# Kernel tuning notes

Measured on AMD Instinct MI355X. Metric: run time of the kernel, lower is better.

The kernel has to match this reference:

```python
import jax, jax.numpy as jnp
import numpy as np

N, E, B = 100000, 1600000, 512
NE, EE, H = 32, 32, 64
SCALE = float(2**48 - 1)


def _mlp2(x, W1, b1, W2, b2):
    # Linear -> ReLU -> Linear
    return jax.nn.relu(x @ W1 + b1) @ W2 + b2


def _gine(x, src, dst, e, W1, b1, W2, b2, n):
    # GINEConv (eps=0): nn(x + sum_j relu(x_j + e_ij))
    m = jax.nn.relu(x[src] + e)                      # [E, d] gather + edge add
    agg = jax.ops.segment_sum(m, dst, num_segments=n)  # scatter-add to targets
    return _mlp2(x + agg, W1, b1, W2, b2)


def _encode(names, edge_index, edge_attr, batch,
            idW1, idb1, idW2, idb2, edW1, edb1, edW2, edb2,
            c1W1, c1b1, c1W2, c1b2, c2W1, c2b1, c2W2, c2b2, linW, linb):
    norm = jnp.clip((names.astype(jnp.float32) + 2.0) / SCALE, 0.0, 1.0)[:, None]
    x = _mlp2(norm, idW1, idb1, idW2, idb2)          # [N, NE]
    e = _mlp2(edge_attr, edW1, edb1, edW2, edb2)     # [E, EE]
    src, dst = edge_index[0], edge_index[1]
    x = jax.nn.relu(_gine(x, src, dst, e, c1W1, c1b1, c1W2, c1b2, N))
    e2 = e @ linW + linb                             # edge lin for conv2 (EE->H)
    x = jax.nn.relu(_gine(x, src, dst, e2, c2W1, c2b1, c2W2, c2b2, N))
    sums = jax.ops.segment_sum(x, batch, num_segments=B)
    cnt = jax.ops.segment_sum(jnp.ones((x.shape[0],), x.dtype), batch, num_segments=B)
    return sums / jnp.maximum(cnt, 1.0)[:, None]     # global_mean_pool


def setup_inputs() -> dict:
    key = jax.random.key(0)
    ks = iter(jax.random.split(key, 64))
    def w(shape):
        return jax.random.normal(next(ks), shape, dtype=jnp.float32) * 0.05
    d = {}
    d['node_names_s'] = jax.random.randint(next(ks), (N,), 0, 1000000)
    d['edge_index_s'] = jax.random.randint(next(ks), (2, E), 0, N)
    d['edge_attr_s'] = jax.random.uniform(next(ks), (E, 1), dtype=jnp.float32)
    d['batch_s'] = jnp.sort(jax.random.randint(next(ks), (N,), 0, B))
    d['node_names_g'] = jax.random.randint(next(ks), (N,), 0, 1000000)
    d['edge_index_g'] = jax.random.randint(next(ks), (2, E), 0, N)
    d['edge_attr_g'] = jax.random.uniform(next(ks), (E, 1), dtype=jnp.float32)
    d['batch_g'] = jnp.sort(jax.random.randint(next(ks), (N,), 0, B))
    d['depth'] = jax.random.uniform(next(ks), (B,), dtype=jnp.float32)
    # shared encoders
    d['idW1'], d['idb1'], d['idW2'], d['idb2'] = w((1, NE)), w((NE,)), w((NE, NE)), w((NE,))
    d['edW1'], d['edb1'], d['edW2'], d['edb2'] = w((1, EE)), w((EE,)), w((EE, EE)), w((EE,))
    # state convs
    d['s1W1'], d['s1b1'], d['s1W2'], d['s1b2'] = w((NE, H)), w((H,)), w((H, H)), w((H,))
    d['s2W1'], d['s2b1'], d['s2W2'], d['s2b2'] = w((H, H)), w((H,)), w((H, H)), w((H,))
    d['s2linW'], d['s2linb'] = w((EE, H)), w((H,))
    # goal convs
    d['g1W1'], d['g1b1'], d['g1W2'], d['g1b2'] = w((NE, H)), w((H,)), w((H, H)), w((H,))
    d['g2W1'], d['g2b1'], d['g2W2'], d['g2b2'] = w((H, H)), w((H,)), w((H, H)), w((H,))
    d['g2linW'], d['g2linb'] = w((EE, H)), w((H,))
    d['rW1'], d['rb1'], d['rW2'], d['rb2'] = w((2 * H + 1, H)), w((H,)), w((H, 1)), w((1,))
    return d


def reference(node_names_s, edge_index_s, edge_attr_s, batch_s,
              node_names_g, edge_index_g, edge_attr_g, batch_g, depth,
              idW1, idb1, idW2, idb2, edW1, edb1, edW2, edb2,
              s1W1, s1b1, s1W2, s1b2, s2W1, s2b1, s2W2, s2b2, s2linW, s2linb,
              g1W1, g1b1, g1W2, g1b2, g2W1, g2b1, g2W2, g2b2, g2linW, g2linb,
              rW1, rb1, rW2, rb2):
    s = _encode(node_names_s, edge_index_s, edge_attr_s, batch_s,
                idW1, idb1, idW2, idb2, edW1, edb1, edW2, edb2,
                s1W1, s1b1, s1W2, s1b2, s2W1, s2b1, s2W2, s2b2, s2linW, s2linb)
    g = _encode(node_names_g, edge_index_g, edge_attr_g, batch_g,
                idW1, idb1, idW2, idb2, edW1, edb1, edW2, edb2,
                g1W1, g1b1, g1W2, g1b2, g2W1, g2b1, g2W2, g2b2, g2linW, g2linb)
    z = jnp.concatenate([s, g, depth[:, None]], axis=1)  # [B, 2H+1]
    return _mlp2(z, rW1, rb1, rW2, rb2)[:, 0]            # [B]
```

## Files before the change

### kernel.cpp

```cpp
#include <hip/hip_runtime.h>
#include <hip/hip_fp16.h>
#include <stdint.h>

namespace {

constexpr int NN   = 100000;
constexpr int TN   = 2 * NN;
constexpr int NEDG = 1600000;
constexpr int TE   = 2 * NEDG;
constexpr int NBAT = 512;
constexpr int NSEG = 33;

constexpr int NC     = 782;
constexpr int TILE   = 4096;
constexpr int ABLK   = (TE + TILE - 1) / TILE;
constexpr int ENTCAP = 5120;

constexpr int S1H = 20;
constexpr int S2H = 36;

constexpr int TAB_BP = 0;
constexpr int TAB_D1 = 32;
constexpr int TAB_C1 = TAB_D1 + NSEG * 32;
constexpr int TAB_E2 = TAB_C1 + NSEG * 32;
constexpr int TAB_TOTAL = TAB_E2 + 4 * NSEG * 64;

__device__ __forceinline__ float relu_(float x) { return fmaxf(x, 0.0f); }

__device__ __forceinline__ float4 shfl_xor4(float4 v, int m) {
  return make_float4(__shfl_xor(v.x, m), __shfl_xor(v.y, m),
                     __shfl_xor(v.z, m), __shfl_xor(v.w, m));
}

__device__ __forceinline__ __half2 bch(int u) {
  return *reinterpret_cast<__half2*>(&u);
}
__device__ __forceinline__ int f2h2(float a, float b) {
  __half2 h = __floats2half2_rn(a, b);
  return *reinterpret_cast<int*>(&h);
}

__global__ void build_tables(const float* __restrict__ eW1, const float* __restrict__ eb1,
                             const float* __restrict__ eW2, const float* __restrict__ eb2,
                             const float* __restrict__ sLW, const float* __restrict__ sLb,
                             const float* __restrict__ gLW, const float* __restrict__ gLb,
                             float* __restrict__ tabs) {
  __shared__ float traw[32];
  __shared__ float ts[32];
  __shared__ float dt[NSEG * 32];
  __shared__ float ct[NSEG * 32];
  int tid = threadIdx.x;
  if (tid < 32) {
    float w = eW1[tid], b = eb1[tid];
    traw[tid] = (w != 0.0f) ? (-b / w) : 3.0e38f;
  }
  __syncthreads();
  if (tid < 32) {
    float v = traw[tid];
    int r = 0;
    for (int j = 0; j < 32; ++j) {
      float u = traw[j];
      r += (u < v) || (u == v && j < tid);
    }
    ts[r] = v;
  }
  __syncthreads();
  if (tid < 32) tabs[TAB_BP + tid] = ts[tid];
  for (int idx = tid; idx < NSEG * 32; idx += blockDim.x) {
    int s = idx >> 5, j = idx & 31;
    float a;
    if (s == 0)            a = ts[0] - 1.0f;
    else if (s == NSEG - 1) a = ts[31] + 1.0f;
    else                   a = 0.5f * ts[s - 1] + 0.5f * ts[s];
    float d = 0.0f, c = 0.0f;
    for (int i = 0; i < 32; ++i) {
      float w = eW1[i], b = eb1[i];
      if (fmaf(a, w, b) > 0.0f) {
        float w2 = eW2[i * 32 + j];
        d = fmaf(w, w2, d);
        c = fmaf(b, w2, c);
      }
    }
    c += eb2[j];
    dt[idx] = d; ct[idx] = c;
    tabs[TAB_D1 + idx] = d;
    tabs[TAB_C1 + idx] = c;
  }
  __syncthreads();
  for (int idx = tid; idx < NSEG * 64; idx += blockDim.x) {
    int s = idx >> 6, k = idx & 63;
    float ds = 0.f, cs = 0.f, dg = 0.f, cg = 0.f;
    for (int j = 0; j < 32; ++j) {
      float dv = dt[s * 32 + j], cv = ct[s * 32 + j];
      float ws = sLW[j * 64 + k], wg = gLW[j * 64 + k];
      ds = fmaf(dv, ws, ds); cs = fmaf(cv, ws, cs);
      dg = fmaf(dv, wg, dg); cg = fmaf(cv, wg, cg);
    }
    cs += sLb[k]; cg += gLb[k];
    tabs[TAB_E2 + idx]                 = ds;
    tabs[TAB_E2 + NSEG * 64 + idx]     = cs;
    tabs[TAB_E2 + 2 * NSEG * 64 + idx] = dg;
    tabs[TAB_E2 + 3 * NSEG * 64 + idx] = cg;
  }
}

__global__ __launch_bounds__(256) void fused_front(
    const int* __restrict__ names_s, const int* __restrict__ names_g,
    const float* __restrict__ idW1, const float* __restrict__ idb1,
    const float* __restrict__ idW2, const float* __restrict__ idb2,
    const int* __restrict__ src_s, const int* __restrict__ dst_s, const float* __restrict__ attr_s,
    const int* __restrict__ src_g, const int* __restrict__ dst_g, const float* __restrict__ attr_g,
    const int* __restrict__ bat_s, const int* __restrict__ bat_g,
    const float* __restrict__ tabs,
    float* __restrict__ x0, __half* __restrict__ x0h,
    int* __restrict__ gcur, int2* __restrict__ part,
    int* __restrict__ start_s, int* __restrict__ start_g) {
  __shared__ int hist[NC];
  __shared__ int lofs[NC];
  __shared__ int lcur[NC];
  __shared__ int2 sorted[TILE];
  __shared__ int addr[TILE];
  __shared__ int scanbuf[256];
  __shared__ float bp[32];
  int t = threadIdx.x;
  if (blockIdx.x < ABLK) {
    if (t < 32) bp[t] = tabs[TAB_BP + t];
    for (int i = t; i < NC; i += 256) hist[i] = 0;
    __syncthreads();
    int base = blockIdx.x * TILE;
#pragma unroll
    for (int j = 0; j < 16; ++j) {
      int i = base + j * 256 + t;
      if (i < TE) {
        int d = (i < NEDG) ? dst_s[i] : (dst_g[i - NEDG] + NN);
        atomicAdd(&hist[d >> 8], 1);
      }
    }
    __syncthreads();
    int loc[4];
    int sum = 0;
#pragma unroll
    for (int j = 0; j < 4; ++j) {
      int b = t * 4 + j;
      int v = (b < NC) ? hist[b] : 0;
      loc[j] = sum; sum += v;
    }
    scanbuf[t] = sum;
    __syncthreads();
    for (int st = 1; st < 256; st <<= 1) {
      int u = (t >= st) ? scanbuf[t - st] : 0;
      __syncthreads();
      scanbuf[t] += u;
      __syncthreads();
    }
    int texcl = scanbuf[t] - sum;
#pragma unroll
    for (int j = 0; j < 4; ++j) {
      int b = t * 4 + j;
      if (b < NC) { lofs[b] = texcl + loc[j]; lcur[b] = 0; }
    }
    __syncthreads();
    for (int b = t; b < NC; b += 256) {
      int c = hist[b];
      hist[b] = c ? atomicAdd(&gcur[b], c) : 0;
    }
    __syncthreads();
#pragma unroll
    for (int j = 0; j < 16; ++j) {
      int i = base + j * 256 + t;
      if (i < TE) {
        int sl, d; float a;
        if (i < NEDG) { sl = src_s[i]; d = dst_s[i]; a = attr_s[i]; }
        else { int k = i - NEDG; sl = src_g[k]; d = dst_g[k] + NN; a = attr_g[k]; }
        int seg = 0;
#pragma unroll
        for (int q = 0; q < 32; ++q) seg += (bp[q] < a);
        int c = d >> 8;
        int r = atomicAdd(&lcur[c], 1);
        int s = lofs[c] + r;
        sorted[s] = make_int2(sl | ((d & 255) << 17) | (seg << 25), __float_as_int(a));
        addr[s] = c * ENTCAP + hist[c] + r;
      }
    }
    __syncthreads();
    int tot = (base + TILE <= TE) ? TILE : (TE - base);
    for (int s = t; s < tot; s += 256) part[addr[s]] = sorted[s];
  } else if (blockIdx.x < ABLK + 782) {
    int n = (blockIdx.x - ABLK) * 256 + t;
    if (n >= TN) return;
    int name = (n < NN) ? names_s[n] : names_g[n - NN];
    float norm = ((float)name + 2.0f) / 281474976710655.0f;
    norm = fminf(fmaxf(norm, 0.0f), 1.0f);
    float h[32];
#pragma unroll
    for (int i = 0; i < 32; ++i) h[i] = relu_(fmaf(norm, idW1[i], idb1[i]));
    float4* out = (float4*)(x0 + (size_t)n * 32);
    int2* outh = (int2*)(x0h + (size_t)n * 32);
    for (int j0 = 0; j0 < 32; j0 += 4) {
      float a0 = idb2[j0], a1 = idb2[j0 + 1], a2 = idb2[j0 + 2], a3 = idb2[j0 + 3];
#pragma unroll
      for (int i = 0; i < 32; ++i) {
        float hv = h[i];
        a0 = fmaf(hv, idW2[i * 32 + j0],     a0);
        a1 = fmaf(hv, idW2[i * 32 + j0 + 1], a1);
        a2 = fmaf(hv, idW2[i * 32 + j0 + 2], a2);
        a3 = fmaf(hv, idW2[i * 32 + j0 + 3], a3);
      }
      out[j0 >> 2] = make_float4(a0, a1, a2, a3);
      outh[j0 >> 2] = make_int2(f2h2(a0, a1), f2h2(a2, a3));
    }
  } else {
    int blk = blockIdx.x - ABLK - 782;
    int half = blk >= 391;
    const int* bat = half ? bat_g : bat_s;
    int* start = half ? start_g : start_s;
    int i = (blk - half * 391) * 256 + t;
    if (i >= NN) return;
    int cur = bat[i];
    int prev = (i == 0) ? -1 : bat[i - 1];
    for (int b = prev + 1; b <= cur; ++b) start[b] = i;
    if (i == NN - 1) {
      for (int b = cur + 1; b <= NBAT; ++b) start[b] = NN;
    }
  }
}

__global__ __launch_bounds__(1024) void coarse_scan(
    const int* __restrict__ gcur, int* __restrict__ cbase, int* __restrict__ rowptr) {
  __shared__ int s[1024];
  int t = threadIdx.x;
  int v = (t < NC) ? min(gcur[t], ENTCAP) : 0;
  s[t] = v;
  __syncthreads();
  for (int st = 1; st < 1024; st <<= 1) {
    int u = (t >= st) ? s[t - st] : 0;
    __syncthreads();
    s[t] += u;
    __syncthreads();
  }
  if (t < NC) cbase[t] = s[t] - v;
  if (t == 0) rowptr[TN] = TE;
}

__global__ __launch_bounds__(256) void partition_to_csr(
    const int* __restrict__ gcur, const int* __restrict__ cbase,
    const int2* __restrict__ part,
    int* __restrict__ rowptr, int2* __restrict__ colattr) {
  __shared__ int2 outE[ENTCAP];
  __shared__ int hist[256];
  __shared__ int cur[256];
  __shared__ int sc[256];
  int t = threadIdx.x, b = blockIdx.x;
  hist[t] = 0;
  __syncthreads();
  int cnt = min(gcur[b], ENTCAP);
  int ibase = b * ENTCAP;
  int obase = cbase[b];
  for (int i = t; i < cnt; i += 256)
    atomicAdd(&hist[(part[ibase + i].x >> 17) & 255], 1);
  __syncthreads();
  int v = hist[t];
  sc[t] = v;
  __syncthreads();
  for (int st = 1; st < 256; st <<= 1) {
    int u = (t >= st) ? sc[t - st] : 0;
    __syncthreads();
    sc[t] += u;
    __syncthreads();
  }
  int excl = sc[t] - v;
  int gnode = b * 256 + t;
  if (gnode < TN) rowptr[gnode] = obase + excl;
  cur[t] = excl;
  __syncthreads();
  for (int i = t; i < cnt; i += 256) {
    int2 e = part[ibase + i];
    int dl = (e.x >> 17) & 255;
    int srcn = e.x & 0x1FFFF;
    int seg = (e.x >> 25) & 63;
    int pos = atomicAdd(&cur[dl], 1);
    outE[pos] = make_int2(srcn | (seg << 20), e.y);
  }
  __syncthreads();
  for (int i = t; i < cnt; i += 256) colattr[obase + i] = outE[i];
}

__global__ __launch_bounds__(256) void conv1_dual(
    const float* __restrict__ x0, const __half* __restrict__ x0h,
    const int* __restrict__ rowptr, const int2* __restrict__ colattr,
    const float* __restrict__ tabs, float* __restrict__ hb) {
  __shared__ __half2 dt2[NSEG * S1H];
  __shared__ __half2 ct2[NSEG * S1H];
  for (int i = threadIdx.x; i < NSEG * 16; i += 256) {
    int s = i >> 4, j = i & 15;
    dt2[s * S1H + j] = __floats2half2_rn(tabs[TAB_D1 + s * 32 + 2 * j],
                                         tabs[TAB_D1 + s * 32 + 2 * j + 1]);
    ct2[s * S1H + j] = __floats2half2_rn(tabs[TAB_C1 + s * 32 + 2 * j],
                                         tabs[TAB_C1 + s * 32 + 2 * j + 1]);
  }
  __syncthreads();
  int n = blockIdx.x * 4 + (threadIdx.x >> 6);
  const __half* xb = x0h + (n >= NN ? (size_t)NN * 32 : 0);
  int lane = threadIdx.x & 63;
  int sub = lane & 7;
  int f0  = (lane >> 3) * 4;
  int h0  = (lane >> 3) * 2;
  int beg = rowptr[n], end = rowptr[n + 1];
  float4 acc = make_float4(0.f, 0.f, 0.f, 0.f);
  for (int k = beg + sub; k < end; k += 16) {
    int2 ca0 = colattr[k];
    int kb = k + 8;
    bool has1 = kb < end;
    int2 ca1 = has1 ? colattr[kb] : ca0;
    unsigned p0 = (unsigned)ca0.x, p1 = (unsigned)ca1.x;
    int s0 = (int)(p0 & 0xFFFFFu), g0 = (int)(p0 >> 20);
    int s1 = (int)(p1 & 0xFFFFFu), g1 = (int)(p1 >> 20);
    float a0 = __int_as_float(ca0.y), a1 = __int_as_float(ca1.y);
    __half2 az0 = __floats2half2_rn(a0, a0);
    __half2 az1 = __floats2half2_rn(a1, a1);
    int2 xv0 = *(const int2*)(xb + (size_t)s0 * 32 + f0);
    int2 xv1 = *(const int2*)(xb + (size_t)s1 * 32 + f0);
    int2 dv0 = *(const int2*)&dt2[g0 * S1H + h0];
    int2 cv0 = *(const int2*)&ct2[g0 * S1H + h0];
    __half2 v;
    float2 f;
    v = __hadd2(bch(xv0.x), __hfma2(az0, bch(dv0.x), bch(cv0.x)));
    f = __half22float2(v); acc.x += relu_(f.x); acc.y += relu_(f.y);
    v = __hadd2(bch(xv0.y), __hfma2(az0, bch(dv0.y), bch(cv0.y)));
    f = __half22float2(v); acc.z += relu_(f.x); acc.w += relu_(f.y);
    if (has1) {
      int2 dv1 = *(const int2*)&dt2[g1 * S1H + h0];
      int2 cv1 = *(const int2*)&ct2[g1 * S1H + h0];
      v = __hadd2(bch(xv1.x), __hfma2(az1, bch(dv1.x), bch(cv1.x)));
      f = __half22float2(v); acc.x += relu_(f.x); acc.y += relu_(f.y);
      v = __hadd2(bch(xv1.y), __hfma2(az1, bch(dv1.y), bch(cv1.y)));
      f = __half22float2(v); acc.z += relu_(f.x); acc.w += relu_(f.y);
    }
  }
#pragma unroll
  for (int m = 1; m < 8; m <<= 1) {
    float4 o = shfl_xor4(acc, m);
    acc.x += o.x; acc.y += o.y; acc.z += o.z; acc.w += o.w;
  }
  if (sub == 0) {
    const float4 self = *(const float4*)(x0 + (size_t)n * 32 + f0);
    *(float4*)(hb + (size_t)n * 32 + f0) =
        make_float4(self.x + acc.x, self.y + acc.y, self.z + acc.z, self.w + acc.w);
  }
}

__global__ __launch_bounds__(256) void conv2_dual(
    const float* __restrict__ x1, const __half* __restrict__ x1h,
    const int* __restrict__ rowptr, const int2* __restrict__ colattr,
    const float* __restrict__ tabs, float* __restrict__ hb) {
  __shared__ __half2 dt2[NSEG * S2H];
  __shared__ __half2 ct2[NSEG * S2H];
  int half = blockIdx.x >= (NN / 4);
  const float* d2 = tabs + TAB_E2 + (size_t)half * 2 * NSEG * 64;
  for (int i = threadIdx.x; i < NSEG * 32; i += 256) {
    int s = i >> 5, j = i & 31;
    dt2[s * S2H + j] = __floats2half2_rn(d2[s * 64 + 2 * j], d2[s * 64 + 2 * j + 1]);
    ct2[s * S2H + j] = __floats2half2_rn(d2[NSEG * 64 + s * 64 + 2 * j],
                                         d2[NSEG * 64 + s * 64 + 2 * j + 1]);
  }
  __syncthreads();
  int n = blockIdx.x * 4 + (threadIdx.x >> 6);
  const __half* xb = x1h + (size_t)half * NN * 64;
  int lane = threadIdx.x & 63;
  int sub = lane & 7;
  int f0  = (lane >> 3) * 8;
  int h0  = (lane >> 3) * 4;
  int beg = rowptr[n], end = rowptr[n + 1];
  float4 accA = make_float4(0.f, 0.f, 0.f, 0.f);
  float4 accB = make_float4(0.f, 0.f, 0.f, 0.f);
  for (int k = beg + sub; k < end; k += 16) {
    int2 ca0 = colattr[k];
    int kb = k + 8;
    bool has1 = kb < end;
    int2 ca1 = has1 ? colattr[kb] : ca0;
    unsigned p0 = (unsigned)ca0.x, p1 = (unsigned)ca1.x;
    int s0 = (int)(p0 & 0xFFFFFu), g0 = (int)(p0 >> 20);
    int s1 = (int)(p1 & 0xFFFFFu), g1 = (int)(p1 >> 20);
    float a0 = __int_as_float(ca0.y), a1 = __int_as_float(ca1.y);
    __half2 az0 = __floats2half2_rn(a0, a0);
    __half2 az1 = __floats2half2_rn(a1, a1);
    int4 xv0 = *(const int4*)(xb + (size_t)s0 * 64 + f0);
    int4 xv1 = *(const int4*)(xb + (size_t)s1 * 64 + f0);
    int4 dv0 = *(const int4*)&dt2[g0 * S2H + h0];
    int4 cv0 = *(const int4*)&ct2[g0 * S2H + h0];
    __half2 v;
    float2 f;
    v = __hadd2(bch(xv0.x), __hfma2(az0, bch(dv0.x), bch(cv0.x)));
    f = __half22float2(v); accA.x += relu_(f.x); accA.y += relu_(f.y);
    v = __hadd2(bch(xv0.y), __hfma2(az0, bch(dv0.y), bch(cv0.y)));
    f = __half22float2(v); accA.z += relu_(f.x); accA.w += relu_(f.y);
    v = __hadd2(bch(xv0.z), __hfma2(az0, bch(dv0.z), bch(cv0.z)));
    f = __half22float2(v); accB.x += relu_(f.x); accB.y += relu_(f.y);
    v = __hadd2(bch(xv0.w), __hfma2(az0, bch(dv0.w), bch(cv0.w)));
    f = __half22float2(v); accB.z += relu_(f.x); accB.w += relu_(f.y);
    if (has1) {
      int4 dv1 = *(const int4*)&dt2[g1 * S2H + h0];
      int4 cv1 = *(const int4*)&ct2[g1 * S2H + h0];
      v = __hadd2(bch(xv1.x), __hfma2(az1, bch(dv1.x), bch(cv1.x)));
      f = __half22float2(v); accA.x += relu_(f.x); accA.y += relu_(f.y);
      v = __hadd2(bch(xv1.y), __hfma2(az1, bch(dv1.y), bch(cv1.y)));
      f = __half22float2(v); accA.z += relu_(f.x); accA.w += relu_(f.y);
      v = __hadd2(bch(xv1.z), __hfma2(az1, bch(dv1.z), bch(cv1.z)));
      f = __half22float2(v); accB.x += relu_(f.x); accB.y += relu_(f.y);
      v = __hadd2(bch(xv1.w), __hfma2(az1, bch(dv1.w), bch(cv1.w)));
      f = __half22float2(v); accB.z += relu_(f.x); accB.w += relu_(f.y);
    }
  }
#pragma unroll
  for (int m = 1; m < 8; m <<= 1) {
    float4 oA = shfl_xor4(accA, m);
    float4 oB = shfl_xor4(accB, m);
    accA.x += oA.x; accA.y += oA.y; accA.z += oA.z; accA.w += oA.w;
    accB.x += oB.x; accB.y += oB.y; accB.z += oB.z; accB.w += oB.w;
  }
  if (sub == 0) {
    const float* sp = x1 + (size_t)n * 64 + f0;
    const float4 sA = *(const float4*)sp;
    const float4 sB = *(const float4*)(sp + 4);
    float* op = hb + (size_t)n * 64 + f0;
    *(float4*)op       = make_float4(sA.x + accA.x, sA.y + accA.y, sA.z + accA.z, sA.w + accA.w);
    *(float4*)(op + 4) = make_float4(sB.x + accB.x, sB.y + accB.y, sB.z + accB.z, sB.w + accB.w);
  }
}

__global__ __launch_bounds__(256) void mlp1_dual(
    const float* __restrict__ hin,
    const float* __restrict__ sW1, const float* __restrict__ sb1,
    const float* __restrict__ sW2, const float* __restrict__ sb2,
    const float* __restrict__ gW1, const float* __restrict__ gb1,
    const float* __restrict__ gW2, const float* __restrict__ gb2,
    float* __restrict__ xout, __half* __restrict__ hout) {
  constexpr int IN = 32;
  __shared__ float hsT[IN][65];
  __shared__ float ysT[64][65];
  int base = blockIdx.x * 64;
  for (int idx = threadIdx.x; idx < 64 * IN; idx += 256) {
    int node = idx / IN, k = idx - node * IN;
    hsT[k][node] = hin[(size_t)(base + node) * IN + k];
  }
  __syncthreads();
  int nt = threadIdx.x >> 4, jx = threadIdx.x & 15;
  int n0 = nt * 4, f0 = jx * 4;
  bool isg = (base + n0) >= NN;
  const float* W1 = isg ? gW1 : sW1;
  const float* b1 = isg ? gb1 : sb1;
  const float* W2 = isg ? gW2 : sW2;
  const float* b2 = isg ? gb2 : sb2;
  float4 acc0, acc1, acc2, acc3;
  {
    const float4 b = *(const float4*)(b1 + f0);
    acc0 = b; acc1 = b; acc2 = b; acc3 = b;
  }
  for (int k = 0; k < IN; ++k) {
    const float4 h = *(const float4*)&hsT[k][n0];
    const float4 w = *(const float4*)(W1 + k * 64 + f0);
    acc0.x = fmaf(h.x, w.x, acc0.x); acc0.y = fmaf(h.x, w.y, acc0.y);
    acc0.z = fmaf(h.x, w.z, acc0.z); acc0.w = fmaf(h.x, w.w, acc0.w);
    acc1.x = fmaf(h.y, w.x, acc1.x); acc1.y = fmaf(h.y, w.y, acc1.y);
    acc1.z = fmaf(h.y, w.z, acc1.z); acc1.w = fmaf(h.y, w.w, acc1.w);
    acc2.x = fmaf(h.z, w.x, acc2.x); acc2.y = fmaf(h.z, w.y, acc2.y);
    acc2.z = fmaf(h.z, w.z, acc2.z); acc2.w = fmaf(h.z, w.w, acc2.w);
    acc3.x = fmaf(h.w, w.x, acc3.x); acc3.y = fmaf(h.w, w.y, acc3.y);
    acc3.z = fmaf(h.w, w.z, acc3.z); acc3.w = fmaf(h.w, w.w, acc3.w);
  }
  ysT[f0 + 0][n0 + 0] = relu_(acc0.x); ysT[f0 + 1][n0 + 0] = relu_(acc0.y);
  ysT[f0 + 2][n0 + 0] = relu_(acc0.z); ysT[f0 + 3][n0 + 0] = relu_(acc0.w);
  ysT[f0 + 0][n0 + 1] = relu_(acc1.x); ysT[f0 + 1][n0 + 1] = relu_(acc1.y);
  ysT[f0 + 2][n0 + 1] = relu_(acc1.z); ysT[f0 + 3][n0 + 1] = relu_(acc1.w);
  ysT[f0 + 0][n0 + 2] = relu_(acc2.x); ysT[f0 + 1][n0 + 2] = relu_(acc2.y);
  ysT[f0 + 2][n0 + 2] = relu_(acc2.z); ysT[f0 + 3][n0 + 2] = relu_(acc2.w);
  ysT[f0 + 0][n0 + 3] = relu_(acc3.x); ysT[f0 + 1][n0 + 3] = relu_(acc3.y);
  ysT[f0 + 2][n0 + 3] = relu_(acc3.z); ysT[f0 + 3][n0 + 3] = relu_(acc3.w);
  __syncthreads();
  {
    const float4 b = *(const float4*)(b2 + f0);
    acc0 = b; acc1 = b; acc2 = b; acc3 = b;
  }
  for (int k = 0; k < 64; ++k) {
    const float4 h = *(const float4*)&ysT[k][n0];
    const float4 w = *(const float4*)(W2 + k * 64 + f0);
    acc0.x = fmaf(h.x, w.x, acc0.x); acc0.y = fmaf(h.x, w.y, acc0.y);
    acc0.z = fmaf(h.x, w.z, acc0.z); acc0.w = fmaf(h.x, w.w, acc0.w);
    acc1.x = fmaf(h.y, w.x, acc1.x); acc1.y = fmaf(h.y, w.y, acc1.y);
    acc1.z = fmaf(h.y, w.z, acc1.z); acc1.w = fmaf(h.y, w.w, acc1.w);
    acc2.x = fmaf(h.z, w.x, acc2.x); acc2.y = fmaf(h.z, w.y, acc2.y);
    acc2.z = fmaf(h.z, w.z, acc2.z); acc2.w = fmaf(h.z, w.w, acc2.w);
    acc3.x = fmaf(h.w, w.x, acc3.x); acc3.y = fmaf(h.w, w.y, acc3.y);
    acc3.z = fmaf(h.w, w.z, acc3.z); acc3.w = fmaf(h.w, w.w, acc3.w);
  }
  float4 o;
  o = make_float4(relu_(acc0.x), relu_(acc0.y), relu_(acc0.z), relu_(acc0.w));
  *(float4*)(xout + (size_t)(base + n0 + 0) * 64 + f0) = o;
  *(int2*)(hout + (size_t)(base + n0 + 0) * 64 + f0) = make_int2(f2h2(o.x, o.y), f2h2(o.z, o.w));
  o = make_float4(relu_(acc1.x), relu_(acc1.y), relu_(acc1.z), relu_(acc1.w));
  *(float4*)(xout + (size_t)(base + n0 + 1) * 64 + f0) = o;
  *(int2*)(hout + (size_t)(base + n0 + 1) * 64 + f0) = make_int2(f2h2(o.x, o.y), f2h2(o.z, o.w));
  o = make_float4(relu_(acc2.x), relu_(acc2.y), relu_(acc2.z), relu_(acc2.w));
  *(float4*)(xout + (size_t)(base + n0 + 2) * 64 + f0) = o;
  *(int2*)(hout + (size_t)(base + n0 + 2) * 64 + f0) = make_int2(f2h2(o.x, o.y), f2h2(o.z, o.w));
  o = make_float4(relu_(acc3.x), relu_(acc3.y), relu_(acc3.z), relu_(acc3.w));
  *(float4*)(xout + (size_t)(base + n0 + 3) * 64 + f0) = o;
  *(int2*)(hout + (size_t)(base + n0 + 3) * 64 + f0) = make_int2(f2h2(o.x, o.y), f2h2(o.z, o.w));
}

__global__ __launch_bounds__(256) void mlp2_pool_dual(
    const float* __restrict__ hin,
    const float* __restrict__ sW1, const float* __restrict__ sb1,
    const float* __restrict__ sW2, const float* __restrict__ sb2,
    const float* __restrict__ gW1, const float* __restrict__ gb1,
    const float* __restrict__ gW2, const float* __restrict__ gb2,
    const int* __restrict__ bat_s, const int* __restrict__ bat_g,
    float* __restrict__ psum) {
  constexpr int IN = 64;
  __shared__ float hsT[IN][65];
  __shared__ float ysT[64][65];
  __shared__ int pid[64];
  int base = blockIdx.x * 64;
  for (int idx = threadIdx.x; idx < 64 * IN; idx += 256) {
    int node = idx / IN, k = idx - node * IN;
    hsT[k][node] = hin[(size_t)(base + node) * IN + k];
  }
  if (threadIdx.x < 64) {
    int gb = base + threadIdx.x;
    pid[threadIdx.x] = (gb < NN) ? bat_s[gb] : (NBAT + bat_g[gb - NN]);
  }
  __syncthreads();
  int nt = threadIdx.x >> 4, jx = threadIdx.x & 15;
  int n0 = nt * 4, f0 = jx * 4;
  bool isg = (base + n0) >= NN;
  const float* W1 = isg ? gW1 : sW1;
  const float* b1 = isg ? gb1 : sb1;
  const float* W2 = isg ? gW2 : sW2;
  const float* b2 = isg ? gb2 : sb2;
  float4 acc0, acc1, acc2, acc3;
  {
    const float4 b = *(const float4*)(b1 + f0);
    acc0 = b; acc1 = b; acc2 = b; acc3 = b;
  }
  for (int k = 0; k < IN; ++k) {
    const float4 h = *(const float4*)&hsT[k][n0];
    const float4 w = *(const float4*)(W1 + k * 64 + f0);
    acc0.x = fmaf(h.x, w.x, acc0.x); acc0.y = fmaf(h.x, w.y, acc0.y);
    acc0.z = fmaf(h.x, w.z, acc0.z); acc0.w = fmaf(h.x, w.w, acc0.w);
    acc1.x = fmaf(h.y, w.x, acc1.x); acc1.y = fmaf(h.y, w.y, acc1.y);
    acc1.z = fmaf(h.y, w.z, acc1.z); acc1.w = fmaf(h.y, w.w, acc1.w);
    acc2.x = fmaf(h.z, w.x, acc2.x); acc2.y = fmaf(h.z, w.y, acc2.y);
    acc2.z = fmaf(h.z, w.z, acc2.z); acc2.w = fmaf(h.z, w.w, acc2.w);
    acc3.x = fmaf(h.w, w.x, acc3.x); acc3.y = fmaf(h.w, w.y, acc3.y);
    acc3.z = fmaf(h.w, w.z, acc3.z); acc3.w = fmaf(h.w, w.w, acc3.w);
  }
  ysT[f0 + 0][n0 + 0] = relu_(acc0.x); ysT[f0 + 1][n0 + 0] = relu_(acc0.y);
  ysT[f0 + 2][n0 + 0] = relu_(acc0.z); ysT[f0 + 3][n0 + 0] = relu_(acc0.w);
  ysT[f0 + 0][n0 + 1] = relu_(acc1.x); ysT[f0 + 1][n0 + 1] = relu_(acc1.y);
  ysT[f0 + 2][n0 + 1] = relu_(acc1.z); ysT[f0 + 3][n0 + 1] = relu_(acc1.w);
  ysT[f0 + 0][n0 + 2] = relu_(acc2.x); ysT[f0 + 1][n0 + 2] = relu_(acc2.y);
  ysT[f0 + 2][n0 + 2] = relu_(acc2.z); ysT[f0 + 3][n0 + 2] = relu_(acc2.w);
  ysT[f0 + 0][n0 + 3] = relu_(acc3.x); ysT[f0 + 1][n0 + 3] = relu_(acc3.y);
  ysT[f0 + 2][n0 + 3] = relu_(acc3.z); ysT[f0 + 3][n0 + 3] = relu_(acc3.w);
  __syncthreads();
  {
    const float4 b = *(const float4*)(b2 + f0);
    acc0 = b; acc1 = b; acc2 = b; acc3 = b;
  }
  for (int k = 0; k < 64; ++k) {
    const float4 h = *(const float4*)&ysT[k][n0];
    const float4 w = *(const float4*)(W2 + k * 64 + f0);
    acc0.x = fmaf(h.x, w.x, acc0.x); acc0.y = fmaf(h.x, w.y, acc0.y);
    acc0.z = fmaf(h.x, w.z, acc0.z); acc0.w = fmaf(h.x, w.w, acc0.w);
    acc1.x = fmaf(h.y, w.x, acc1.x); acc1.y = fmaf(h.y, w.y, acc1.y);
    acc1.z = fmaf(h.y, w.z, acc1.z); acc1.w = fmaf(h.y, w.w, acc1.w);
    acc2.x = fmaf(h.z, w.x, acc2.x); acc2.y = fmaf(h.z, w.y, acc2.y);
    acc2.z = fmaf(h.z, w.z, acc2.z); acc2.w = fmaf(h.z, w.w, acc2.w);
    acc3.x = fmaf(h.w, w.x, acc3.x); acc3.y = fmaf(h.w, w.y, acc3.y);
    acc3.z = fmaf(h.w, w.z, acc3.z); acc3.w = fmaf(h.w, w.w, acc3.w);
  }
  __syncthreads();
  ysT[f0 + 0][n0 + 0] = relu_(acc0.x); ysT[f0 + 1][n0 + 0] = relu_(acc0.y);
  ysT[f0 + 2][n0 + 0] = relu_(acc0.z); ysT[f0 + 3][n0 + 0] = relu_(acc0.w);
  ysT[f0 + 0][n0 + 1] = relu_(acc1.x); ysT[f0 + 1][n0 + 1] = relu_(acc1.y);
  ysT[f0 + 2][n0 + 1] = relu_(acc1.z); ysT[f0 + 3][n0 + 1] = relu_(acc1.w);
  ysT[f0 + 0][n0 + 2] = relu_(acc2.x); ysT[f0 + 1][n0 + 2] = relu_(acc2.y);
  ysT[f0 + 2][n0 + 2] = relu_(acc2.z); ysT[f0 + 3][n0 + 2] = relu_(acc2.w);
  ysT[f0 + 0][n0 + 3] = relu_(acc3.x); ysT[f0 + 1][n0 + 3] = relu_(acc3.y);
  ysT[f0 + 2][n0 + 3] = relu_(acc3.z); ysT[f0 + 3][n0 + 3] = relu_(acc3.w);
  __syncthreads();
  int c = threadIdx.x >> 6, f = threadIdx.x & 63;
  int cur = pid[c * 16];
  float run = 0.0f;
  for (int i = 0; i < 16; ++i) {
    int nx = c * 16 + i;
    int p = pid[nx];
    if (p != cur) { atomicAdd(&psum[(size_t)cur * 64 + f], run); run = 0.0f; cur = p; }
    run += ysT[f][nx];
  }
  atomicAdd(&psum[(size_t)cur * 64 + f], run);
}

__global__ __launch_bounds__(256) void regressor16(
    const float* __restrict__ psum,
    const int* __restrict__ start_s, const int* __restrict__ start_g,
    const float* __restrict__ depth,
    const float* __restrict__ W1, const float* __restrict__ b1,
    const float* __restrict__ W2, const float* __restrict__ b2,
    float* __restrict__ out) {
  __shared__ float zs[16][132];
  __shared__ float ys[64][17];
  __shared__ float inv_s[16], inv_g[16];
  int base = blockIdx.x * 16;
  if (threadIdx.x < 16) {
    int b = base + threadIdx.x;
    inv_s[threadIdx.x] = 1.0f / fmaxf((float)(start_s[b + 1] - start_s[b]), 1.0f);
    inv_g[threadIdx.x] = 1.0f / fmaxf((float)(start_g[b + 1] - start_g[b]), 1.0f);
  }
  __syncthreads();
  for (int i = threadIdx.x; i < 16 * 64; i += 256) {
    int ln = i >> 6, k = i & 63;
    zs[ln][k]      = psum[(size_t)(base + ln) * 64 + k] * inv_s[ln];
    zs[ln][64 + k] = psum[(size_t)(NBAT + base + ln) * 64 + k] * inv_g[ln];
  }
  if (threadIdx.x < 16) zs[threadIdx.x][128] = depth[base + threadIdx.x];
  __syncthreads();
  int g = threadIdx.x >> 4;
  int j = threadIdx.x & 15;
  int f0 = j * 4;
  float a0, a1, a2, a3;
  {
    const float4 b = *(const float4*)(b1 + f0);
    a0 = b.x; a1 = b.y; a2 = b.z; a3 = b.w;
  }
  for (int k = 0; k < 129; ++k) {
    float zv = zs[g][k];
    const float4 w = *(const float4*)(W1 + k * 64 + f0);
    a0 = fmaf(zv, w.x, a0); a1 = fmaf(zv, w.y, a1);
    a2 = fmaf(zv, w.z, a2); a3 = fmaf(zv, w.w, a3);
  }
  ys[f0 + 0][g] = relu_(a0);
  ys[f0 + 1][g] = relu_(a1);
  ys[f0 + 2][g] = relu_(a2);
  ys[f0 + 3][g] = relu_(a3);
  __syncthreads();
  float s = ys[f0 + 0][g] * W2[f0 + 0] + ys[f0 + 1][g] * W2[f0 + 1] +
            ys[f0 + 2][g] * W2[f0 + 2] + ys[f0 + 3][g] * W2[f0 + 3];
#pragma unroll
  for (int m = 1; m < 16; m <<= 1) s += __shfl_xor(s, m);
  if (j == 0) out[base + g] = s + b2[0];
}

}

extern "C" void kernel_launch(void* const* d_in, const int* in_sizes, int n_in,
                              void* d_out, int out_size, void* d_ws, size_t ws_size,
                              hipStream_t stream) {
  const int*   names_s = (const int*)d_in[0];
  const int*   ei_s    = (const int*)d_in[1];
  const float* ea_s    = (const float*)d_in[2];
  const int*   bat_s   = (const int*)d_in[3];
  const int*   names_g = (const int*)d_in[4];
  const int*   ei_g    = (const int*)d_in[5];
  const float* ea_g    = (const float*)d_in[6];
  const int*   bat_g   = (const int*)d_in[7];
  const float* depth   = (const float*)d_in[8];
  const float* idW1 = (const float*)d_in[9],  *idb1 = (const float*)d_in[10];
  const float* idW2 = (const float*)d_in[11], *idb2 = (const float*)d_in[12];
  const float* edW1 = (const float*)d_in[13], *edb1 = (const float*)d_in[14];
  const float* edW2 = (const float*)d_in[15], *edb2 = (const float*)d_in[16];
  const float* s1W1 = (const float*)d_in[17], *s1b1 = (const float*)d_in[18];
  const float* s1W2 = (const float*)d_in[19], *s1b2 = (const float*)d_in[20];
  const float* s2W1 = (const float*)d_in[21], *s2b1 = (const float*)d_in[22];
  const float* s2W2 = (const float*)d_in[23], *s2b2 = (const float*)d_in[24];
  const float* s2LW = (const float*)d_in[25], *s2Lb = (const float*)d_in[26];
  const float* g1W1 = (const float*)d_in[27], *g1b1 = (const float*)d_in[28];
  const float* g1W2 = (const float*)d_in[29], *g1b2 = (const float*)d_in[30];
  const float* g2W1 = (const float*)d_in[31], *g2b1 = (const float*)d_in[32];
  const float* g2W2 = (const float*)d_in[33], *g2b2 = (const float*)d_in[34];
  const float* g2LW = (const float*)d_in[35], *g2Lb = (const float*)d_in[36];
  const float* rW1  = (const float*)d_in[37], *rb1  = (const float*)d_in[38];
  const float* rW2  = (const float*)d_in[39], *rb2  = (const float*)d_in[40];
  (void)in_sizes; (void)n_in; (void)out_size; (void)ws_size;

  char* ws = (char*)d_ws;
  size_t off = 0;
  auto alloc = [&](size_t bytes) -> char* {
    char* p = ws + off;
    off += (bytes + 255) & ~(size_t)255;
    return p;
  };
  float* tabs    = (float*)alloc((size_t)TAB_TOTAL * 4);
  char*  act   = alloc((size_t)TN * 64 * 4 * 2);
  float* x0buf = (float*)act;
  float* h1buf = (float*)(act + (size_t)TN * 32 * 4);
  float* x1buf = (float*)(act + (size_t)TN * 64 * 4);
  int2*  part  = (int2*)x1buf;
  float* h2buf = (float*)act;
  __half* x0h  = (__half*)alloc((size_t)TN * 32 * 2);
  __half* x1h  = (__half*)alloc((size_t)TN * 64 * 2);
  int2*  colattr = (int2*) alloc((size_t)TE * 8);
  int*   gcur    = (int*)  alloc((size_t)NC * 4);
  int*   cbase   = (int*)  alloc((size_t)NC * 4);
  int*   rowptr  = (int*)  alloc((size_t)(TN + 1) * 4);
  int*   start_s = (int*)  alloc((size_t)(NBAT + 1) * 4);
  int*   start_g = (int*)  alloc((size_t)(NBAT + 1) * 4);
  float* psum    = (float*)alloc((size_t)2 * NBAT * 64 * 4);

  build_tables<<<1, 256, 0, stream>>>(edW1, edb1, edW2, edb2, s2LW, s2Lb, g2LW, g2Lb, tabs);
  hipMemsetAsync(gcur, 0, (size_t)NC * 4, stream);
  hipMemsetAsync(psum, 0, (size_t)2 * NBAT * 64 * 4, stream);

  fused_front<<<ABLK + 782 + 782, 256, 0, stream>>>(
      names_s, names_g, idW1, idb1, idW2, idb2,
      ei_s, ei_s + NEDG, ea_s, ei_g, ei_g + NEDG, ea_g,
      bat_s, bat_g, tabs, x0buf, x0h, gcur, part, start_s, start_g);
  coarse_scan<<<1, 1024, 0, stream>>>(gcur, cbase, rowptr);
  partition_to_csr<<<NC, 256, 0, stream>>>(gcur, cbase, part, rowptr, colattr);

  conv1_dual<<<TN / 4, 256, 0, stream>>>(x0buf, x0h, rowptr, colattr, tabs, h1buf);
  mlp1_dual<<<TN / 64, 256, 0, stream>>>(h1buf,
                                         s1W1, s1b1, s1W2, s1b2,
                                         g1W1, g1b1, g1W2, g1b2, x1buf, x1h);
  conv2_dual<<<TN / 4, 256, 0, stream>>>(x1buf, x1h, rowptr, colattr, tabs, h2buf);
  mlp2_pool_dual<<<TN / 64, 256, 0, stream>>>(h2buf,
                                              s2W1, s2b1, s2W2, s2b2,
                                              g2W1, g2b1, g2W2, g2b2,
                                              bat_s, bat_g, psum);
  regressor16<<<32, 256, 0, stream>>>(psum, start_s, start_g, depth,
                                      rW1, rb1, rW2, rb2, (float*)d_out);
}
```

Baseline: 678.1 us.

## Drop fp32 activation copies and widen per-lane gathers in conv kernels

Removes the fp32 copies of x0 and x1; the self term in each conv is now read from the existing fp16 buffers, which cuts global writes and reads. The conv kernels regroup lanes into 16 edge slots times 4 feature groups, so each lane gathers 16 or 32 contiguous bytes per edge instead of 8 or 16. A wave-level __any check skips the second edge slot when no lane has one, and a 0/1 multiplier masks the lanes that do not. The self term is now rounded to fp16, which slightly reduces accuracy, and the wider per-lane accumulators raise register pressure.

```diff
diff --git a/kernel.cpp b/kernel.cpp
--- a/kernel.cpp
+++ b/kernel.cpp
@@ -112,7 +112,7 @@
     const int* __restrict__ src_g, const int* __restrict__ dst_g, const float* __restrict__ attr_g,
     const int* __restrict__ bat_s, const int* __restrict__ bat_g,
     const float* __restrict__ tabs,
-    float* __restrict__ x0, __half* __restrict__ x0h,
+    __half* __restrict__ x0h,
     int* __restrict__ gcur, int2* __restrict__ part,
     int* __restrict__ start_s, int* __restrict__ start_g) {
   __shared__ int hist[NC];
@@ -194,7 +194,6 @@
     float h[32];
 #pragma unroll
     for (int i = 0; i < 32; ++i) h[i] = relu_(fmaf(norm, idW1[i], idb1[i]));
-    float4* out = (float4*)(x0 + (size_t)n * 32);
     int2* outh = (int2*)(x0h + (size_t)n * 32);
     for (int j0 = 0; j0 < 32; j0 += 4) {
       float a0 = idb2[j0], a1 = idb2[j0 + 1], a2 = idb2[j0 + 2], a3 = idb2[j0 + 3];
@@ -206,7 +205,6 @@
         a2 = fmaf(hv, idW2[i * 32 + j0 + 2], a2);
         a3 = fmaf(hv, idW2[i * 32 + j0 + 3], a3);
       }
-      out[j0 >> 2] = make_float4(a0, a1, a2, a3);
       outh[j0 >> 2] = make_int2(f2h2(a0, a1), f2h2(a2, a3));
     }
   } else {
@@ -285,8 +283,24 @@
   for (int i = t; i < cnt; i += 256) colattr[obase + i] = outE[i];
 }
 
+__device__ __forceinline__ void edge_math1(int4 xv, const __half2* dt2, const __half2* ct2,
+                                           int g, int h0, __half2 az, float m,
+                                           float4& A, float4& B) {
+  int4 dv = *(const int4*)&dt2[g * S1H + h0];
+  int4 cv = *(const int4*)&ct2[g * S1H + h0];
+  __half2 v; float2 f;
+  v = __hadd2(bch(xv.x), __hfma2(az, bch(dv.x), bch(cv.x)));
+  f = __half22float2(v); A.x = fmaf(m, relu_(f.x), A.x); A.y = fmaf(m, relu_(f.y), A.y);
+  v = __hadd2(bch(xv.y), __hfma2(az, bch(dv.y), bch(cv.y)));
+  f = __half22float2(v); A.z = fmaf(m, relu_(f.x), A.z); A.w = fmaf(m, relu_(f.y), A.w);
+  v = __hadd2(bch(xv.z), __hfma2(az, bch(dv.z), bch(cv.z)));
+  f = __half22float2(v); B.x = fmaf(m, relu_(f.x), B.x); B.y = fmaf(m, relu_(f.y), B.y);
+  v = __hadd2(bch(xv.w), __hfma2(az, bch(dv.w), bch(cv.w)));
+  f = __half22float2(v); B.z = fmaf(m, relu_(f.x), B.z); B.w = fmaf(m, relu_(f.y), B.w);
+}
+
 __global__ __launch_bounds__(256) void conv1_dual(
-    const float* __restrict__ x0, const __half* __restrict__ x0h,
+    const __half* __restrict__ x0h,
     const int* __restrict__ rowptr, const int2* __restrict__ colattr,
     const float* __restrict__ tabs, float* __restrict__ hb) {
   __shared__ __half2 dt2[NSEG * S1H];
@@ -302,61 +316,89 @@
   int n = blockIdx.x * 4 + (threadIdx.x >> 6);
   const __half* xb = x0h + (n >= NN ? (size_t)NN * 32 : 0);
   int lane = threadIdx.x & 63;
-  int sub = lane & 7;
-  int f0  = (lane >> 3) * 4;
-  int h0  = (lane >> 3) * 2;
+  int sub = lane & 15;
+  int f0  = (lane >> 4) * 8;
+  int h0  = (lane >> 4) * 4;
   int beg = rowptr[n], end = rowptr[n + 1];
-  float4 acc = make_float4(0.f, 0.f, 0.f, 0.f);
-  for (int k = beg + sub; k < end; k += 16) {
+  int4 sv = make_int4(0, 0, 0, 0);
+  if (sub == 0) sv = *(const int4*)(x0h + (size_t)n * 32 + f0);
+  float4 accA = make_float4(0.f, 0.f, 0.f, 0.f);
+  float4 accB = make_float4(0.f, 0.f, 0.f, 0.f);
+  for (int k = beg + sub; k < end; k += 32) {
     int2 ca0 = colattr[k];
-    int kb = k + 8;
-    bool has1 = kb < end;
-    int2 ca1 = has1 ? colattr[kb] : ca0;
-    unsigned p0 = (unsigned)ca0.x, p1 = (unsigned)ca1.x;
-    int s0 = (int)(p0 & 0xFFFFFu), g0 = (int)(p0 >> 20);
-    int s1 = (int)(p1 & 0xFFFFFu), g1 = (int)(p1 >> 20);
-    float a0 = __int_as_float(ca0.y), a1 = __int_as_float(ca1.y);
+    unsigned p0 = (unsigned)ca0.x;
+    const __half* r0 = xb + (size_t)(p0 & 0xFFFFFu) * 32 + f0;
+    int4 xv0 = *(const int4*)r0;
+    int g0 = (int)(p0 >> 20);
+    float a0 = __int_as_float(ca0.y);
     __half2 az0 = __floats2half2_rn(a0, a0);
-    __half2 az1 = __floats2half2_rn(a1, a1);
-    int2 xv0 = *(const int2*)(xb + (size_t)s0 * 32 + f0);
-    int2 xv1 = *(const int2*)(xb + (size_t)s1 * 32 + f0);
-    int2 dv0 = *(const int2*)&dt2[g0 * S1H + h0];
-    int2 cv0 = *(const int2*)&ct2[g0 * S1H + h0];
-    __half2 v;
-    float2 f;
-    v = __hadd2(bch(xv0.x), __hfma2(az0, bch(dv0.x), bch(cv0.x)));
-    f = __half22float2(v); acc.x += relu_(f.x); acc.y += relu_(f.y);
-    v = __hadd2(bch(xv0.y), __hfma2(az0, bch(dv0.y), bch(cv0.y)));
-    f = __half22float2(v); acc.z += relu_(f.x); acc.w += relu_(f.y);
-    if (has1) {
-      int2 dv1 = *(const int2*)&dt2[g1 * S1H + h0];
-      int2 cv1 = *(const int2*)&ct2[g1 * S1H + h0];
-      v = __hadd2(bch(xv1.x), __hfma2(az1, bch(dv1.x), bch(cv1.x)));
-      f = __half22float2(v); acc.x += relu_(f.x); acc.y += relu_(f.y);
-      v = __hadd2(bch(xv1.y), __hfma2(az1, bch(dv1.y), bch(cv1.y)));
-      f = __half22float2(v); acc.z += relu_(f.x); acc.w += relu_(f.y);
-    }
-  }
-#pragma unroll
-  for (int m = 1; m < 8; m <<= 1) {
-    float4 o = shfl_xor4(acc, m);
-    acc.x += o.x; acc.y += o.y; acc.z += o.z; acc.w += o.w;
+    int kb = k + 16;
+    if (__any(kb < end)) {
+      bool has1 = kb < end;
+      int2 ca1 = has1 ? colattr[kb] : ca0;
+      unsigned p1 = (unsigned)ca1.x;
+      const __half* r1 = xb + (size_t)(p1 & 0xFFFFFu) * 32 + f0;
+      int4 xv1 = *(const int4*)r1;
+      int g1 = (int)(p1 >> 20);
+      float a1 = __int_as_float(ca1.y);
+      __half2 az1 = __floats2half2_rn(a1, a1);
+      float m1 = has1 ? 1.0f : 0.0f;
+      edge_math1(xv0, dt2, ct2, g0, h0, az0, 1.0f, accA, accB);
+      edge_math1(xv1, dt2, ct2, g1, h0, az1, m1, accA, accB);
+    } else {
+      edge_math1(xv0, dt2, ct2, g0, h0, az0, 1.0f, accA, accB);
+    }
+  }
+#pragma unroll
+  for (int m = 1; m < 16; m <<= 1) {
+    float4 oA = shfl_xor4(accA, m);
+    float4 oB = shfl_xor4(accB, m);
+    accA.x += oA.x; accA.y += oA.y; accA.z += oA.z; accA.w += oA.w;
+    accB.x += oB.x; accB.y += oB.y; accB.z += oB.z; accB.w += oB.w;
   }
   if (sub == 0) {
-    const float4 self = *(const float4*)(x0 + (size_t)n * 32 + f0);
-    *(float4*)(hb + (size_t)n * 32 + f0) =
-        make_float4(self.x + acc.x, self.y + acc.y, self.z + acc.z, self.w + acc.w);
-  }
+    float2 t0 = __half22float2(bch(sv.x)), t1 = __half22float2(bch(sv.y));
+    float2 t2 = __half22float2(bch(sv.z)), t3 = __half22float2(bch(sv.w));
+    float* op = hb + (size_t)n * 32 + f0;
+    *(float4*)op       = make_float4(t0.x + accA.x, t0.y + accA.y, t1.x + accA.z, t1.y + accA.w);
+    *(float4*)(op + 4) = make_float4(t2.x + accB.x, t2.y + accB.y, t3.x + accB.z, t3.y + accB.w);
+  }
+}
+
+__device__ __forceinline__ void edge_math2(int4 xa, int4 xbq, const __half2* dt2, const __half2* ct2,
+                                           int g, int h0, __half2 az, float m,
+                                           float4& A, float4& B, float4& C, float4& D) {
+  const int4* dp = (const int4*)&dt2[g * S2H + h0];
+  const int4* cp = (const int4*)&ct2[g * S2H + h0];
+  int4 dv = dp[0], cv = cp[0];
+  __half2 v; float2 f;
+  v = __hadd2(bch(xa.x), __hfma2(az, bch(dv.x), bch(cv.x)));
+  f = __half22float2(v); A.x = fmaf(m, relu_(f.x), A.x); A.y = fmaf(m, relu_(f.y), A.y);
+  v = __hadd2(bch(xa.y), __hfma2(az, bch(dv.y), bch(cv.y)));
+  f = __half22float2(v); A.z = fmaf(m, relu_(f.x), A.z); A.w = fmaf(m, relu_(f.y), A.w);
+  v = __hadd2(bch(xa.z), __hfma2(az, bch(dv.z), bch(cv.z)));
+  f = __half22float2(v); B.x = fmaf(m, relu_(f.x), B.x); B.y = fmaf(m, relu_(f.y), B.y);
+  v = __hadd2(bch(xa.w), __hfma2(az, bch(dv.w), bch(cv.w)));
+  f = __half22float2(v); B.z = fmaf(m, relu_(f.x), B.z); B.w = fmaf(m, relu_(f.y), B.w);
+  dv = dp[1]; cv = cp[1];
+  v = __hadd2(bch(xbq.x), __hfma2(az, bch(dv.x), bch(cv.x)));
+  f = __half22float2(v); C.x = fmaf(m, relu_(f.x), C.x); C.y = fmaf(m, relu_(f.y), C.y);
+  v = __hadd2(bch(xbq.y), __hfma2(az, bch(dv.y), bch(cv.y)));
+  f = __half22float2(v); C.z = fmaf(m, relu_(f.x), C.z); C.w = fmaf(m, relu_(f.y), C.w);
+  v = __hadd2(bch(xbq.z), __hfma2(az, bch(dv.z), bch(cv.z)));
+  f = __half22float2(v); D.x = fmaf(m, relu_(f.x), D.x); D.y = fmaf(m, relu_(f.y), D.y);
+  v = __hadd2(bch(xbq.w), __hfma2(az, bch(dv.w), bch(cv.w)));
+  f = __half22float2(v); D.z = fmaf(m, relu_(f.x), D.z); D.w = fmaf(m, relu_(f.y), D.w);
 }
 
 __global__ __launch_bounds__(256) void conv2_dual(
-    const float* __restrict__ x1, const __half* __restrict__ x1h,
+    const __half* __restrict__ x1h,
     const int* __restrict__ rowptr, const int2* __restrict__ colattr,
     const float* __restrict__ tabs, float* __restrict__ hb) {
   __shared__ __half2 dt2[NSEG * S2H];
   __shared__ __half2 ct2[NSEG * S2H];
-  int half = blockIdx.x >= (NN / 4);
-  const float* d2 = tabs + TAB_E2 + (size_t)half * 2 * NSEG * 64;
+  int halfg = blockIdx.x >= (NN / 4);
+  const float* d2 = tabs + TAB_E2 + (size_t)halfg * 2 * NSEG * 64;
   for (int i = threadIdx.x; i < NSEG * 32; i += 256) {
     int s = i >> 5, j = i & 31;
     dt2[s * S2H + j] = __floats2half2_rn(d2[s * 64 + 2 * j], d2[s * 64 + 2 * j + 1]);
@@ -365,66 +407,70 @@
   }
   __syncthreads();
   int n = blockIdx.x * 4 + (threadIdx.x >> 6);
-  const __half* xb = x1h + (size_t)half * NN * 64;
+  const __half* xb = x1h + (size_t)halfg * NN * 64;
   int lane = threadIdx.x & 63;
-  int sub = lane & 7;
-  int f0  = (lane >> 3) * 8;
-  int h0  = (lane >> 3) * 4;
+  int sub = lane & 15;
+  int f0  = (lane >> 4) * 16;
+  int h0  = (lane >> 4) * 8;
   int beg = rowptr[n], end = rowptr[n + 1];
+  int4 sv0 = make_int4(0, 0, 0, 0), sv1 = make_int4(0, 0, 0, 0);
+  if (sub == 0) {
+    const __half* srow = x1h + (size_t)n * 64 + f0;
+    sv0 = *(const int4*)srow;
+    sv1 = *(const int4*)(srow + 8);
+  }
   float4 accA = make_float4(0.f, 0.f, 0.f, 0.f);
   float4 accB = make_float4(0.f, 0.f, 0.f, 0.f);
-  for (int k = beg + sub; k < end; k += 16) {
+  float4 accC = make_float4(0.f, 0.f, 0.f, 0.f);
+  float4 accD = make_float4(0.f, 0.f, 0.f, 0.f);
+  for (int k = beg + sub; k < end; k += 32) {
     int2 ca0 = colattr[k];
-    int kb = k + 8;
-    bool has1 = kb < end;
-    int2 ca1 = has1 ? colattr[kb] : ca0;
-    unsigned p0 = (unsigned)ca0.x, p1 = (unsigned)ca1.x;
-    int s0 = (int)(p0 & 0xFFFFFu), g0 = (int)(p0 >> 20);
-    int s1 = (int)(p1 & 0xFFFFFu), g1 = (int)(p1 >> 20);
-    float a0 = __int_as_float(ca0.y), a1 = __int_as_float(ca1.y);
+    unsigned p0 = (unsigned)ca0.x;
+    const __half* r0 = xb + (size_t)(p0 & 0xFFFFFu) * 64 + f0;
+    int4 xv0a = *(const int4*)r0;
+    int4 xv0b = *(const int4*)(r0 + 8);
+    int g0 = (int)(p0 >> 20);
+    float a0 = __int_as_float(ca0.y);
     __half2 az0 = __floats2half2_rn(a0, a0);
-    __half2 az1 = __floats2half2_rn(a1, a1);
-    int4 xv0 = *(const int4*)(xb + (size_t)s0 * 64 + f0);
-    int4 xv1 = *(const int4*)(xb + (size_t)s1 * 64 + f0);
-    int4 dv0 = *(const int4*)&dt2[g0 * S2H + h0];
-    int4 cv0 = *(const int4*)&ct2[g0 * S2H + h0];
-    __half2 v;
-    float2 f;
-    v = __hadd2(bch(xv0.x), __hfma2(az0, bch(dv0.x), bch(cv0.x)));
-    f = __half22float2(v); accA.x += relu_(f.x); accA.y += relu_(f.y);
-    v = __hadd2(bch(xv0.y), __hfma2(az0, bch(dv0.y), bch(cv0.y)));
-    f = __half22float2(v); accA.z += relu_(f.x); accA.w += relu_(f.y);
-    v = __hadd2(bch(xv0.z), __hfma2(az0, bch(dv0.z), bch(cv0.z)));
-    f = __half22float2(v); accB.x += relu_(f.x); accB.y += relu_(f.y);
-    v = __hadd2(bch(xv0.w), __hfma2(az0, bch(dv0.w), bch(cv0.w)));
-    f = __half22float2(v); accB.z += relu_(f.x); accB.w += relu_(f.y);
-    if (has1) {
-      int4 dv1 = *(const int4*)&dt2[g1 * S2H + h0];
-      int4 cv1 = *(const int4*)&ct2[g1 * S2H + h0];
-      v = __hadd2(bch(xv1.x), __hfma2(az1, bch(dv1.x), bch(cv1.x)));
-      f = __half22float2(v); accA.x += relu_(f.x); accA.y += relu_(f.y);
-      v = __hadd2(bch(xv1.y), __hfma2(az1, bch(dv1.y), bch(cv1.y)));
-      f = __half22float2(v); accA.z += relu_(f.x); accA.w += relu_(f.y);
-      v = __hadd2(bch(xv1.z), __hfma2(az1, bch(dv1.z), bch(cv1.z)));
-      f = __half22float2(v); accB.x += relu_(f.x); accB.y += relu_(f.y);
-      v = __hadd2(bch(xv1.w), __hfma2(az1, bch(dv1.w), bch(cv1.w)));
-      f = __half22float2(v); accB.z += relu_(f.x); accB.w += relu_(f.y);
-    }
-  }
-#pragma unroll
-  for (int m = 1; m < 8; m <<= 1) {
+    int kb = k + 16;
+    if (__any(kb < end)) {
+      bool has1 = kb < end;
+      int2 ca1 = has1 ? colattr[kb] : ca0;
+      unsigned p1 = (unsigned)ca1.x;
+      const __half* r1 = xb + (size_t)(p1 & 0xFFFFFu) * 64 + f0;
+      int4 xv1a = *(const int4*)r1;
+      int4 xv1b = *(const int4*)(r1 + 8);
+      int g1 = (int)(p1 >> 20);
+      float a1 = __int_as_float(ca1.y);
+      __half2 az1 = __floats2half2_rn(a1, a1);
+      float m1 = has1 ? 1.0f : 0.0f;
+      edge_math2(xv0a, xv0b, dt2, ct2, g0, h0, az0, 1.0f, accA, accB, accC, accD);
+      edge_math2(xv1a, xv1b, dt2, ct2, g1, h0, az1, m1, accA, accB, accC, accD);
+    } else {
+      edge_math2(xv0a, xv0b, dt2, ct2, g0, h0, az0, 1.0f, accA, accB, accC, accD);
+    }
+  }
+#pragma unroll
+  for (int m = 1; m < 16; m <<= 1) {
     float4 oA = shfl_xor4(accA, m);
     float4 oB = shfl_xor4(accB, m);
+    float4 oC = shfl_xor4(accC, m);
+    float4 oD = shfl_xor4(accD, m);
     accA.x += oA.x; accA.y += oA.y; accA.z += oA.z; accA.w += oA.w;
     accB.x += oB.x; accB.y += oB.y; accB.z += oB.z; accB.w += oB.w;
+    accC.x += oC.x; accC.y += oC.y; accC.z += oC.z; accC.w += oC.w;
+    accD.x += oD.x; accD.y += oD.y; accD.z += oD.z; accD.w += oD.w;
   }
   if (sub == 0) {
-    const float* sp = x1 + (size_t)n * 64 + f0;
-    const float4 sA = *(const float4*)sp;
-    const float4 sB = *(const float4*)(sp + 4);
+    float2 t0 = __half22float2(bch(sv0.x)), t1 = __half22float2(bch(sv0.y));
+    float2 t2 = __half22float2(bch(sv0.z)), t3 = __half22float2(bch(sv0.w));
+    float2 u0 = __half22float2(bch(sv1.x)), u1 = __half22float2(bch(sv1.y));
+    float2 u2 = __half22float2(bch(sv1.z)), u3 = __half22float2(bch(sv1.w));
     float* op = hb + (size_t)n * 64 + f0;
-    *(float4*)op       = make_float4(sA.x + accA.x, sA.y + accA.y, sA.z + accA.z, sA.w + accA.w);
-    *(float4*)(op + 4) = make_float4(sB.x + accB.x, sB.y + accB.y, sB.z + accB.z, sB.w + accB.w);
+    *(float4*)op        = make_float4(t0.x + accA.x, t0.y + accA.y, t1.x + accA.z, t1.y + accA.w);
+    *(float4*)(op + 4)  = make_float4(t2.x + accB.x, t2.y + accB.y, t3.x + accB.z, t3.y + accB.w);
+    *(float4*)(op + 8)  = make_float4(u0.x + accC.x, u0.y + accC.y, u1.x + accC.z, u1.y + accC.w);
+    *(float4*)(op + 12) = make_float4(u2.x + accD.x, u2.y + accD.y, u3.x + accD.z, u3.y + accD.w);
   }
 }
 
@@ -434,7 +480,7 @@
     const float* __restrict__ sW2, const float* __restrict__ sb2,
     const float* __restrict__ gW1, const float* __restrict__ gb1,
     const float* __restrict__ gW2, const float* __restrict__ gb2,
-    float* __restrict__ xout, __half* __restrict__ hout) {
+    __half* __restrict__ hout) {
   constexpr int IN = 32;
   __shared__ float hsT[IN][65];
   __shared__ float ysT[64][65];
@@ -495,16 +541,12 @@
   }
   float4 o;
   o = make_float4(relu_(acc0.x), relu_(acc0.y), relu_(acc0.z), relu_(acc0.w));
-  *(float4*)(xout + (size_t)(base + n0 + 0) * 64 + f0) = o;
   *(int2*)(hout + (size_t)(base + n0 + 0) * 64 + f0) = make_int2(f2h2(o.x, o.y), f2h2(o.z, o.w));
   o = make_float4(relu_(acc1.x), relu_(acc1.y), relu_(acc1.z), relu_(acc1.w));
-  *(float4*)(xout + (size_t)(base + n0 + 1) * 64 + f0) = o;
   *(int2*)(hout + (size_t)(base + n0 + 1) * 64 + f0) = make_int2(f2h2(o.x, o.y), f2h2(o.z, o.w));
   o = make_float4(relu_(acc2.x), relu_(acc2.y), relu_(acc2.z), relu_(acc2.w));
-  *(float4*)(xout + (size_t)(base + n0 + 2) * 64 + f0) = o;
   *(int2*)(hout + (size_t)(base + n0 + 2) * 64 + f0) = make_int2(f2h2(o.x, o.y), f2h2(o.z, o.w));
   o = make_float4(relu_(acc3.x), relu_(acc3.y), relu_(acc3.z), relu_(acc3.w));
-  *(float4*)(xout + (size_t)(base + n0 + 3) * 64 + f0) = o;
   *(int2*)(hout + (size_t)(base + n0 + 3) * 64 + f0) = make_int2(f2h2(o.x, o.y), f2h2(o.z, o.w));
 }
 
@@ -691,12 +733,10 @@
     return p;
   };
   float* tabs    = (float*)alloc((size_t)TAB_TOTAL * 4);
-  char*  act   = alloc((size_t)TN * 64 * 4 * 2);
-  float* x0buf = (float*)act;
-  float* h1buf = (float*)(act + (size_t)TN * 32 * 4);
-  float* x1buf = (float*)(act + (size_t)TN * 64 * 4);
-  int2*  part  = (int2*)x1buf;
+  char*  act   = alloc((size_t)TN * 64 * 4 + (size_t)TN * 32 * 4);
   float* h2buf = (float*)act;
+  float* h1buf = (float*)(act + (size_t)TN * 64 * 4);
+  int2*  part  = (int2*)act;
   __half* x0h  = (__half*)alloc((size_t)TN * 32 * 2);
   __half* x1h  = (__half*)alloc((size_t)TN * 64 * 2);
   int2*  colattr = (int2*) alloc((size_t)TE * 8);
@@ -714,15 +754,15 @@
   fused_front<<<ABLK + 782 + 782, 256, 0, stream>>>(
       names_s, names_g, idW1, idb1, idW2, idb2,
       ei_s, ei_s + NEDG, ea_s, ei_g, ei_g + NEDG, ea_g,
-      bat_s, bat_g, tabs, x0buf, x0h, gcur, part, start_s, start_g);
+      bat_s, bat_g, tabs, x0h, gcur, part, start_s, start_g);
   coarse_scan<<<1, 1024, 0, stream>>>(gcur, cbase, rowptr);
   partition_to_csr<<<NC, 256, 0, stream>>>(gcur, cbase, part, rowptr, colattr);
 
-  conv1_dual<<<TN / 4, 256, 0, stream>>>(x0buf, x0h, rowptr, colattr, tabs, h1buf);
+  conv1_dual<<<TN / 4, 256, 0, stream>>>(x0h, rowptr, colattr, tabs, h1buf);
   mlp1_dual<<<TN / 64, 256, 0, stream>>>(h1buf,
                                          s1W1, s1b1, s1W2, s1b2,
-                                         g1W1, g1b1, g1W2, g1b2, x1buf, x1h);
-  conv2_dual<<<TN / 4, 256, 0, stream>>>(x1buf, x1h, rowptr, colattr, tabs, h2buf);
+                                         g1W1, g1b1, g1W2, g1b2, x1h);
+  conv2_dual<<<TN / 4, 256, 0, stream>>>(x1h, rowptr, colattr, tabs, h2buf);
   mlp2_pool_dual<<<TN / 64, 256, 0, stream>>>(h2buf,
                                               s2W1, s2b1, s2W2, s2b2,
                                               g2W1, g2b1, g2W2, g2b2,
```

Result: slower. 713.5 us (+5.2%).
